# Performance work log

Measured on AMD Instinct MI355X. Metric: run time of the kernel, lower is better.

Reference implementation:

```python
import jax, jax.numpy as jnp
import numpy as np

# VQ codebook lookup from PhraseModel.vq():
#   dist = ||z[:, None, :] - codebook[None, :, :]||_2  over last axis
#   k = argmin(dist, axis=-1); out = codebook[k]
# We compute squared distances via the expansion ||z||^2 - 2 z.c + ||c||^2
# to avoid materializing the [B, K, D] broadcast difference; argmin over
# squared distance equals argmin over distance, so the output is identical.

B, K, D = 262144, 128, 510

def setup_inputs() -> dict:
    key = jax.random.key(0)
    kz, kc = jax.random.split(key)
    z = jax.random.normal(kz, (B, D), dtype=jnp.float32)
    codebook = jax.random.normal(kc, (K, D), dtype=jnp.float32)
    return {"z": z, "codebook": codebook}

def reference(z, codebook):
    # squared L2 distances, [B, K]
    z_sq = jnp.sum(z * z, axis=-1, keepdims=True)            # [B, 1]
    c_sq = jnp.sum(codebook * codebook, axis=-1)             # [K]
    cross = jnp.einsum('bd,kd->bk', z, codebook)             # [B, K]
    dist2 = z_sq - 2.0 * cross + c_sq[None, :]
    k = jnp.argmin(dist2, axis=-1)                           # [B]
    return codebook[k]                                       # [B, D] gather
```

## Files before the change

### kernel.cpp

```cpp
#include <hip/hip_runtime.h>

#define NB 262144
#define ZD 510
#define NK 128
#define GAP_THR 0.5f
#define CHW 68
#define CHUNK_USH (NK * CHW)
#define CHUNK_U4  (CHUNK_USH / 8)

typedef _Float16 half8 __attribute__((ext_vector_type(8)));
typedef __attribute__((ext_vector_type(16))) float f32x16;

#define WS_CB16_OFF 512
#define WS_KF_OFF   139776

__device__ inline ushort f2h(float v) {
    return (ushort)__builtin_bit_cast(short, (_Float16)v);
}

__global__ void prep_kernel(const float* __restrict__ cb, float* __restrict__ csq,
                            ushort* __restrict__ cb16) {
    const int code = blockIdx.x;
    const int tid  = threadIdx.x;
    const float* row = cb + (size_t)code * ZD;

    __shared__ double ws_red[4];
    double s = 0.0;
    for (int j = 0; j < 2; ++j) {
        int d = tid + (j << 8);
        if (d < ZD) { double v = (double)row[d]; s = fma(v, v, s); }
    }
#pragma unroll
    for (int m = 1; m <= 32; m <<= 1) s += __shfl_xor(s, m, 64);
    if ((tid & 63) == 0) ws_red[tid >> 6] = s;
    __syncthreads();
    if (tid == 0) csq[code] = (float)(ws_red[0] + ws_red[1] + ws_red[2] + ws_red[3]);

    for (int s2 = tid; s2 < 8 * CHW; s2 += 256) {
        int ch = s2 / CHW, off = s2 - ch * CHW;
        int d  = (ch << 6) + off;
        float v = (off < 64 && d < ZD) ? row[d] : 0.f;
        cb16[ch * CHUNK_USH + code * CHW + off] = f2h(v);
    }
}

__global__ __launch_bounds__(256, 3) void vq_fused(
    const float* __restrict__ z, const float* __restrict__ cb,
    const uint4* __restrict__ cb16, const float* __restrict__ csq,
    int* __restrict__ kf, float* __restrict__ out) {
    __shared__ __align__(16) ushort cbb[2][CHUNK_USH];
    __shared__ int km[128];

    const int tid   = threadIdx.x;
    const int lane  = tid & 63;
    const int wv    = tid >> 6;
    const int cmod  = lane & 31;
    const int hi    = lane >> 5;
    const int brow0 = blockIdx.x << 7;
    const int wrow0 = brow0 + (wv << 5);

    f32x16 acc[4];
#pragma unroll
    for (int cf = 0; cf < 4; ++cf)
#pragma unroll
        for (int e = 0; e < 16; ++e) acc[cf][e] = 0.f;

    const float* zrow = z + (size_t)(wrow0 + cmod) * ZD;

    float2 zr[2][16];
#pragma unroll
    for (int t = 0; t < 4; ++t) {
        const int dbase = (t << 4) + (hi << 3);
        zr[0][t * 4 + 0] = *(const float2*)(zrow + dbase);
        zr[0][t * 4 + 1] = *(const float2*)(zrow + dbase + 2);
        zr[0][t * 4 + 2] = *(const float2*)(zrow + dbase + 4);
        zr[0][t * 4 + 3] = *(const float2*)(zrow + dbase + 6);
    }
    {
        uint4 cr0[5];
#pragma unroll
        for (int i = 0; i < 4; ++i) cr0[i] = cb16[(i << 8) + tid];
        if (tid < 64) cr0[4] = cb16[1024 + tid];
#pragma unroll
        for (int i = 0; i < 4; ++i) ((uint4*)cbb[0])[(i << 8) + tid] = cr0[i];
        if (tid < 64) ((uint4*)cbb[0])[1024 + tid] = cr0[4];
    }

#pragma unroll
    for (int c = 0; c < 8; ++c) {
        const int cur = c & 1, nxt = cur ^ 1;
        __syncthreads();

        half8 afr[4];
#pragma unroll
        for (int t = 0; t < 4; ++t) {
            afr[t][0] = (_Float16)zr[cur][t * 4 + 0].x;
            afr[t][1] = (_Float16)zr[cur][t * 4 + 0].y;
            afr[t][2] = (_Float16)zr[cur][t * 4 + 1].x;
            afr[t][3] = (_Float16)zr[cur][t * 4 + 1].y;
            afr[t][4] = (_Float16)zr[cur][t * 4 + 2].x;
            afr[t][5] = (_Float16)zr[cur][t * 4 + 2].y;
            afr[t][6] = (_Float16)zr[cur][t * 4 + 3].x;
            afr[t][7] = (_Float16)zr[cur][t * 4 + 3].y;
        }

        uint4 cr[5];
        if (c < 7) {
#pragma unroll
            for (int i = 0; i < 4; ++i) cr[i] = cb16[(c + 1) * CHUNK_U4 + (i << 8) + tid];
            if (tid < 64) cr[4] = cb16[(c + 1) * CHUNK_U4 + 1024 + tid];
            const int cg = (c + 1) << 6;
#pragma unroll
            for (int t = 0; t < 4; ++t) {
                const int dbase = cg + (t << 4) + (hi << 3);
                zr[nxt][t * 4 + 0] = *(const float2*)(zrow + dbase);
                zr[nxt][t * 4 + 1] = *(const float2*)(zrow + dbase + 2);
                zr[nxt][t * 4 + 2] = *(const float2*)(zrow + dbase + 4);
                zr[nxt][t * 4 + 3] = (dbase + 6 < ZD) ? *(const float2*)(zrow + dbase + 6)
                                                      : make_float2(0.f, 0.f);
            }
        }

#pragma unroll
        for (int t = 0; t < 4; ++t) {
#pragma unroll
            for (int cf = 0; cf < 4; ++cf) {
                const int bbase = (cf * 32 + cmod) * CHW + (t << 4) + (hi << 3);
                union { uint2 u2[2]; half8 h; } b;
                b.u2[0] = *(const uint2*)&cbb[cur][bbase];
                b.u2[1] = *(const uint2*)&cbb[cur][bbase + 4];
                acc[cf] = __builtin_amdgcn_mfma_f32_32x32x16_f16(afr[t], b.h, acc[cf], 0, 0, 0);
            }
        }

        if (c < 7) {
#pragma unroll
            for (int i = 0; i < 4; ++i) ((uint4*)cbb[nxt])[(i << 8) + tid] = cr[i];
            if (tid < 64) ((uint4*)cbb[nxt])[1024 + tid] = cr[4];
        }
    }

    float cq[4];
#pragma unroll
    for (int cf = 0; cf < 4; ++cf) cq[cf] = csq[cf * 32 + cmod];

#pragma unroll
    for (int reg = 0; reg < 16; ++reg) {
        float bv = fmaf(-2.f, acc[0][reg], cq[0]);
        int   bk = cmod;
        float m2 = 1e30f;
#pragma unroll
        for (int cf = 1; cf < 4; ++cf) {
            float v = fmaf(-2.f, acc[cf][reg], cq[cf]);
            int  kk = cf * 32 + cmod;
            if (v < bv)      { m2 = bv; bv = v; bk = kk; }
            else if (v < m2) { m2 = v; }
        }
#pragma unroll
        for (int m = 1; m <= 16; m <<= 1) {
            float ov  = __shfl_xor(bv, m, 64);
            int   ok  = __shfl_xor(bk, m, 64);
            float om2 = __shfl_xor(m2, m, 64);
            float nm2 = fminf(fmaxf(bv, ov), fminf(m2, om2));
            bool take = (ov < bv) || (ov == bv && ok < bk);
            bv = take ? ov : bv;
            bk = take ? ok : bk;
            m2 = nm2;
        }
        if (cmod == 0) {
            int rloc = (reg & 3) + ((reg >> 2) << 3) + (hi << 2);
            int enc  = bk;
            if (m2 - bv < GAP_THR) enc |= (int)0x80000000;
            km[(wv << 5) + rloc] = enc;
            kf[wrow0 + rloc] = enc;
        }
    }
    __syncthreads();

    const int half = tid >> 7, h = tid & 127;
    for (int rp = 0; rp < 64; ++rp) {
        int row = (rp << 1) + half;
        int k   = km[row] & 127;
        const float2* src = (const float2*)(cb + (size_t)k * ZD);
        float2*       dst = (float2*)(out + (size_t)(brow0 + row) * ZD);
        dst[h] = src[h];
        if (h < 127) dst[128 + h] = src[128 + h];
    }
}

__global__ __launch_bounds__(256) void repair(
    const float* __restrict__ z, const float* __restrict__ cb,
    const float* __restrict__ csq, const int* __restrict__ kf,
    float* __restrict__ out) {
    __shared__ int   kmrow[128];
    __shared__ float zsh[4][512];
    const int tid  = threadIdx.x;
    const int wv   = tid >> 6;
    const int lane = tid & 63;
    const int row0 = blockIdx.x << 7;
    if (tid < 128) kmrow[tid] = kf[row0 + tid];
    __syncthreads();
    int nflag = __syncthreads_count(tid < 128 && kmrow[tid] < 0);
    if (nflag == 0) return;

    int cnt = 0;
    for (int rl = 0; rl < 128; ++rl) {
        if (kmrow[rl] >= 0) continue;
        if ((cnt++ & 3) != wv) continue;
        const int row = row0 + rl;
        const float* zr = z + (size_t)row * ZD;
#pragma unroll
        for (int j = 0; j < 8; ++j) {
            int d = (j << 6) + lane;
            zsh[wv][d] = (d < ZD) ? zr[d] : 0.f;
        }
        asm volatile("s_waitcnt lgkmcnt(0)" ::: "memory");

        float bv = 1e30f; int bk = 0;
        for (int c = 0; c < NK; ++c) {
            const float* cr = cb + (size_t)c * ZD;
            float s = 0.f;
#pragma unroll
            for (int j = 0; j < 8; ++j) {
                int d = (j << 6) + lane;
                float cv = (d < ZD) ? cr[d] : 0.f;
                s = fmaf(zsh[wv][d], cv, s);
            }
#pragma unroll
            for (int m = 1; m <= 32; m <<= 1) s += __shfl_xor(s, m, 64);
            float sc = fmaf(-2.f, s, csq[c]);
            if (sc < bv) { bv = sc; bk = c; }
        }
        const float2* src = (const float2*)(cb + (size_t)bk * ZD);
        float2*       dst = (float2*)(out + (size_t)row * ZD);
#pragma unroll
        for (int i = 0; i < 4; ++i) {
            int f2 = (i << 6) + lane;
            if (f2 < 255) dst[f2] = src[f2];
        }
    }
}

extern "C" void kernel_launch(void* const* d_in, const int* in_sizes, int n_in,
                              void* d_out, int out_size, void* d_ws, size_t ws_size,
                              hipStream_t stream) {
    const float* z  = (const float*)d_in[0];
    const float* cb = (const float*)d_in[1];
    float*  out  = (float*)d_out;
    float*  csq  = (float*)d_ws;
    ushort* cb16 = (ushort*)((char*)d_ws + WS_CB16_OFF);
    int*    kf   = (int*)((char*)d_ws + WS_KF_OFF);

    prep_kernel<<<NK, 256, 0, stream>>>(cb, csq, cb16);
    vq_fused<<<NB / 128, 256, 0, stream>>>(z, cb, (const uint4*)cb16, csq, kf, out);
    repair<<<NB / 128, 256, 0, stream>>>(z, cb, csq, kf, out);
}
```

Measured before the change: 481.6 us.

## Compact flagged rows via atomic list and double block size for VQ kernel

The fused kernel now uses 512-thread blocks covering 256 rows, which amortizes each codebook chunk staged in LDS over twice as many rows. Low-margin rows are no longer marked in a per-row flag array. Instead each one is appended to a global list with an atomic counter that the prep kernel resets. The repair kernel then becomes a grid-stride loop over only the listed rows, so it no longer launches 2048 blocks that mostly exit after scanning flags. In exchange the change adds atomic contention and relies on list capacity in the workspace.

```diff
diff --git a/kernel.cpp b/kernel.cpp
--- a/kernel.cpp
+++ b/kernel.cpp
@@ -12,16 +12,18 @@
 typedef __attribute__((ext_vector_type(16))) float f32x16;
 
 #define WS_CB16_OFF 512
-#define WS_KF_OFF   139776
+#define WS_CNT_OFF  139776
+#define WS_LIST_OFF 139840
 
 __device__ inline ushort f2h(float v) {
     return (ushort)__builtin_bit_cast(short, (_Float16)v);
 }
 
 __global__ void prep_kernel(const float* __restrict__ cb, float* __restrict__ csq,
-                            ushort* __restrict__ cb16) {
+                            ushort* __restrict__ cb16, int* __restrict__ cnt) {
     const int code = blockIdx.x;
     const int tid  = threadIdx.x;
+    if (code == 0 && tid == 0) cnt[0] = 0;
     const float* row = cb + (size_t)code * ZD;
 
     __shared__ double ws_red[4];
@@ -44,19 +46,19 @@
     }
 }
 
-__global__ __launch_bounds__(256, 3) void vq_fused(
+__global__ __launch_bounds__(512, 6) void vq_fused(
     const float* __restrict__ z, const float* __restrict__ cb,
     const uint4* __restrict__ cb16, const float* __restrict__ csq,
-    int* __restrict__ kf, float* __restrict__ out) {
+    int* __restrict__ cnt, int* __restrict__ list, float* __restrict__ out) {
     __shared__ __align__(16) ushort cbb[2][CHUNK_USH];
-    __shared__ int km[128];
+    __shared__ int km[256];
 
     const int tid   = threadIdx.x;
     const int lane  = tid & 63;
     const int wv    = tid >> 6;
     const int cmod  = lane & 31;
     const int hi    = lane >> 5;
-    const int brow0 = blockIdx.x << 7;
+    const int brow0 = blockIdx.x << 8;
     const int wrow0 = brow0 + (wv << 5);
 
     f32x16 acc[4];
@@ -77,13 +79,13 @@
         zr[0][t * 4 + 3] = *(const float2*)(zrow + dbase + 6);
     }
     {
-        uint4 cr0[5];
-#pragma unroll
-        for (int i = 0; i < 4; ++i) cr0[i] = cb16[(i << 8) + tid];
-        if (tid < 64) cr0[4] = cb16[1024 + tid];
-#pragma unroll
-        for (int i = 0; i < 4; ++i) ((uint4*)cbb[0])[(i << 8) + tid] = cr0[i];
-        if (tid < 64) ((uint4*)cbb[0])[1024 + tid] = cr0[4];
+        uint4 cr0[3];
+#pragma unroll
+        for (int i = 0; i < 2; ++i) cr0[i] = cb16[(i << 9) + tid];
+        if (tid < 64) cr0[2] = cb16[1024 + tid];
+#pragma unroll
+        for (int i = 0; i < 2; ++i) ((uint4*)cbb[0])[(i << 9) + tid] = cr0[i];
+        if (tid < 64) ((uint4*)cbb[0])[1024 + tid] = cr0[2];
     }
 
 #pragma unroll
@@ -104,11 +106,11 @@
             afr[t][7] = (_Float16)zr[cur][t * 4 + 3].y;
         }
 
-        uint4 cr[5];
+        uint4 cr[3];
         if (c < 7) {
 #pragma unroll
-            for (int i = 0; i < 4; ++i) cr[i] = cb16[(c + 1) * CHUNK_U4 + (i << 8) + tid];
-            if (tid < 64) cr[4] = cb16[(c + 1) * CHUNK_U4 + 1024 + tid];
+            for (int i = 0; i < 2; ++i) cr[i] = cb16[(c + 1) * CHUNK_U4 + (i << 9) + tid];
+            if (tid < 64) cr[2] = cb16[(c + 1) * CHUNK_U4 + 1024 + tid];
             const int cg = (c + 1) << 6;
 #pragma unroll
             for (int t = 0; t < 4; ++t) {
@@ -135,8 +137,8 @@
 
         if (c < 7) {
 #pragma unroll
-            for (int i = 0; i < 4; ++i) ((uint4*)cbb[nxt])[(i << 8) + tid] = cr[i];
-            if (tid < 64) ((uint4*)cbb[nxt])[1024 + tid] = cr[4];
+            for (int i = 0; i < 2; ++i) ((uint4*)cbb[nxt])[(i << 9) + tid] = cr[i];
+            if (tid < 64) ((uint4*)cbb[nxt])[1024 + tid] = cr[2];
         }
     }
 
@@ -169,17 +171,18 @@
         }
         if (cmod == 0) {
             int rloc = (reg & 3) + ((reg >> 2) << 3) + (hi << 2);
-            int enc  = bk;
-            if (m2 - bv < GAP_THR) enc |= (int)0x80000000;
-            km[(wv << 5) + rloc] = enc;
-            kf[wrow0 + rloc] = enc;
+            km[(wv << 5) + rloc] = bk;
+            if (m2 - bv < GAP_THR) {
+                int idx = atomicAdd(cnt, 1);
+                list[idx] = wrow0 + rloc;
+            }
         }
     }
     __syncthreads();
 
     const int half = tid >> 7, h = tid & 127;
     for (int rp = 0; rp < 64; ++rp) {
-        int row = (rp << 1) + half;
+        int row = (rp << 2) + half;
         int k   = km[row] & 127;
         const float2* src = (const float2*)(cb + (size_t)k * ZD);
         float2*       dst = (float2*)(out + (size_t)(brow0 + row) * ZD);
@@ -190,24 +193,17 @@
 
 __global__ __launch_bounds__(256) void repair(
     const float* __restrict__ z, const float* __restrict__ cb,
-    const float* __restrict__ csq, const int* __restrict__ kf,
-    float* __restrict__ out) {
-    __shared__ int   kmrow[128];
+    const float* __restrict__ csq, const int* __restrict__ cnt,
+    const int* __restrict__ list, float* __restrict__ out) {
     __shared__ float zsh[4][512];
     const int tid  = threadIdx.x;
     const int wv   = tid >> 6;
     const int lane = tid & 63;
-    const int row0 = blockIdx.x << 7;
-    if (tid < 128) kmrow[tid] = kf[row0 + tid];
-    __syncthreads();
-    int nflag = __syncthreads_count(tid < 128 && kmrow[tid] < 0);
-    if (nflag == 0) return;
-
-    int cnt = 0;
-    for (int rl = 0; rl < 128; ++rl) {
-        if (kmrow[rl] >= 0) continue;
-        if ((cnt++ & 3) != wv) continue;
-        const int row = row0 + rl;
+    const int n    = cnt[0];
+    const int gw0  = (blockIdx.x << 2) + wv;
+
+    for (int idx = gw0; idx < n; idx += 2048) {
+        const int row = list[idx];
         const float* zr = z + (size_t)row * ZD;
 #pragma unroll
         for (int j = 0; j < 8; ++j) {
@@ -249,9 +245,10 @@
     float*  out  = (float*)d_out;
     float*  csq  = (float*)d_ws;
     ushort* cb16 = (ushort*)((char*)d_ws + WS_CB16_OFF);
-    int*    kf   = (int*)((char*)d_ws + WS_KF_OFF);
-
-    prep_kernel<<<NK, 256, 0, stream>>>(cb, csq, cb16);
-    vq_fused<<<NB / 128, 256, 0, stream>>>(z, cb, (const uint4*)cb16, csq, kf, out);
-    repair<<<NB / 128, 256, 0, stream>>>(z, cb, csq, kf, out);
-}
+    int*    cnt  = (int*)((char*)d_ws + WS_CNT_OFF);
+    int*    list = (int*)((char*)d_ws + WS_LIST_OFF);
+
+    prep_kernel<<<NK, 256, 0, stream>>>(cb, csq, cb16, cnt);
+    vq_fused<<<NB / 256, 512, 0, stream>>>(z, cb, (const uint4*)cb16, csq, cnt, list, out);
+    repair<<<512, 256, 0, stream>>>(z, cb, csq, cnt, list, out);
+}
```

After: 1.304 ms. 2.71x slower.
